# Performance work log

Hardware: AMD Instinct MI355X
Metric: run time of the kernel (lower is better)

Reference implementation:

```python
import jax, jax.numpy as jnp
import numpy as np

B, C, H, W = 8, 192, 56, 56
OUT, K = 192, 9
BN_EPS = 1e-5


def _l2_normalize(x, axis):
    # matches torch F.normalize: x / max(||x||, eps)
    n = jnp.sqrt(jnp.sum(x * x, axis=axis, keepdims=True))
    return x / jnp.maximum(n, 1e-12)


def _knn_idx(x_bnc, k):
    # dense pairwise squared distances, then k nearest (includes self)
    sq = jnp.sum(x_bnc * x_bnc, axis=-1, keepdims=True)            # (b,n,1)
    dist = sq - 2.0 * jnp.einsum('bnc,bmc->bnm', x_bnc, x_bnc) + jnp.swapaxes(sq, 1, 2)
    _, idx = jax.lax.top_k(-dist, k)                                # (b,n,k)
    return idx


def setup_inputs() -> dict:
    key = jax.random.key(0)
    k1, k2 = jax.random.split(key)
    fan_in = 2 * C
    return {
        'x': jax.random.normal(k1, (B, C, H, W), dtype=jnp.float32),
        'conv_w': jax.random.normal(k2, (OUT, 2 * C), dtype=jnp.float32) * np.sqrt(2.0 / fan_in),
        'conv_b': jnp.zeros((OUT,), dtype=jnp.float32),
        'bn_gamma': jnp.ones((OUT,), dtype=jnp.float32),
        'bn_beta': jnp.zeros((OUT,), dtype=jnp.float32),
    }


def reference(x, conv_w, conv_b, bn_gamma, bn_beta):
    b, c, h, w = x.shape
    n = h * w
    xf = x.reshape(b, c, n)                      # (b,c,n) node features
    xt = jnp.swapaxes(xf, 1, 2)                  # (b,n,c)

    # graph build on L2-normalized features (torch does this under no_grad)
    xn = _l2_normalize(xt, axis=-1)
    idx = _knn_idx(jax.lax.stop_gradient(xn), K)  # (b,n,K) neighbor ids

    # gather neighbors; center gather is identity (center_idx == arange)
    x_j = jnp.take_along_axis(xt[:, :, None, :], idx[..., None], axis=1)  # (b,n,K,c)
    x_i = xt[:, :, None, :]                                               # (b,n,1,c)
    feat = jnp.concatenate([jnp.broadcast_to(x_i, x_j.shape), x_j - x_i], axis=-1)  # (b,n,K,2c)

    # 1x1 conv == per-edge linear
    y = jnp.einsum('bnke,oe->bnko', feat, conv_w) + conv_b                # (b,n,K,out)

    # BatchNorm2d (training-mode batch stats over b,n,K per channel)
    mean = jnp.mean(y, axis=(0, 1, 2))
    var = jnp.var(y, axis=(0, 1, 2))
    y = (y - mean) * jax.lax.rsqrt(var + BN_EPS) * bn_gamma + bn_beta

    y = jax.nn.gelu(y, approximate=False)
    y = jnp.max(y, axis=2)                        # max over K neighbors -> (b,n,out)
    return jnp.transpose(y, (0, 2, 1)).reshape(b, -1, h, w)
```

## Files before the change

### kernel.cpp

```cpp
#include <hip/hip_runtime.h>
#include <hip/hip_bf16.h>
#include <math.h>

#define BB 8
#define CC 192
#define HH 56
#define WW 56
#define NPTS 3136
#define OUTC 192
#define KNN 9
#define NTILES 49
#define NCH 2
#define NT4 98
#define NBLK4 (NT4 * BB)

typedef __bf16 bf16x8 __attribute__((ext_vector_type(8)));
typedef float  f32x16 __attribute__((ext_vector_type(16)));

__device__ __forceinline__ unsigned short f2bf(float f) {
    unsigned u = __float_as_uint(f);
    u += 0x7fffu + ((u >> 16) & 1u);
    return (unsigned short)(u >> 16);
}
__device__ __forceinline__ float bf2f(unsigned short h) {
    return __uint_as_float(((unsigned)h) << 16);
}
__device__ __forceinline__ float gelu_f(float z) {
    return 0.5f * z * (1.0f + erff(z * 0.70710678118654752f));
}

__device__ __forceinline__ void ins12u32(unsigned (&t)[12], unsigned key) {
    if (key >= t[11]) return;
    t[11] = key;
#pragma unroll
    for (int q = 11; q > 0; --q) {
        const unsigned a = t[q-1], bq = t[q];
        const bool sw = bq < a;
        t[q-1] = sw ? bq : a;
        t[q]   = sw ? a : bq;
    }
}

__device__ __forceinline__ void ins12u(unsigned long long (&t)[12], unsigned long long key) {
    if (key >= t[11]) return;
    t[11] = key;
#pragma unroll
    for (int q = 11; q > 0; --q) {
        const unsigned long long a = t[q-1], bq = t[q];
        const bool sw = bq < a;
        t[q-1] = sw ? bq : a;
        t[q]   = sw ? a : bq;
    }
}

__device__ __forceinline__ void ins9f(float (&d)[9], int (&ix)[9], float nd, int ni) {
    if (!((nd < d[8]) || (nd == d[8] && ni < ix[8]))) return;
    d[8] = nd; ix[8] = ni;
#pragma unroll
    for (int q = 8; q > 0; --q) {
        if ((d[q] < d[q-1]) || (d[q] == d[q-1] && ix[q] < ix[q-1])) {
            float t = d[q]; d[q] = d[q-1]; d[q-1] = t;
            int t2 = ix[q]; ix[q] = ix[q-1]; ix[q-1] = t2;
        }
    }
}

__global__ __launch_bounds__(256) void k1_normalize(const float* __restrict__ x,
                                                    float* __restrict__ xn,
                                                    unsigned short* __restrict__ xh,
                                                    unsigned short* __restrict__ xl,
                                                    float* __restrict__ normv,
                                                    float* __restrict__ sqv) {
    const int b  = blockIdx.y;
    const int n0 = blockIdx.x * 64;
    __shared__ float tile[64 * 193];
    __shared__ float red[4][64];
    __shared__ float inv[64];
    const int tid = threadIdx.x;
    const int p   = tid & 63;
    const int cg  = tid >> 6;
    const float* xb = x + (size_t)b * CC * NPTS;

    float acc = 0.f;
#pragma unroll 4
    for (int t = 0; t < 48; ++t) {
        const int c = cg * 48 + t;
        const float v = xb[(size_t)c * NPTS + n0 + p];
        tile[p * 193 + c] = v;
        acc += v * v;
    }
    red[cg][p] = acc;
    __syncthreads();
    if (cg == 0) {
        const float s  = red[0][p] + red[1][p] + red[2][p] + red[3][p];
        float nc = sqrtf(s);
        nc = fmaxf(nc, 1e-12f);
        normv[b * NPTS + n0 + p] = nc;
        const float iv = 1.0f / nc;
        inv[p] = iv;
        sqv[b * NPTS + n0 + p] = s * iv * iv;
    }
    __syncthreads();
    const size_t base = ((size_t)b * NPTS + n0) * CC;
    float* dst = xn + base;
    for (int q = tid; q < 64 * CC / 4; q += 256) {
        const int f   = q * 4;
        const int row = f / CC;
        const int c   = f - row * CC;
        const float iv = inv[row];
        float4 v;
        v.x = tile[row * 193 + c + 0] * iv;
        v.y = tile[row * 193 + c + 1] * iv;
        v.z = tile[row * 193 + c + 2] * iv;
        v.w = tile[row * 193 + c + 3] * iv;
        *(float4*)&dst[f] = v;
        ushort4 hv, lv;
        hv.x = f2bf(v.x); lv.x = f2bf(v.x - bf2f(hv.x));
        hv.y = f2bf(v.y); lv.y = f2bf(v.y - bf2f(hv.y));
        hv.z = f2bf(v.z); lv.z = f2bf(v.z - bf2f(hv.z));
        hv.w = f2bf(v.w); lv.w = f2bf(v.w - bf2f(hv.w));
        *(ushort4*)&xh[base + f] = hv;
        *(ushort4*)&xl[base + f] = lv;
    }
}

__global__ __launch_bounds__(256, 3) void k2_knn(const unsigned short* __restrict__ xh,
                                                 const unsigned short* __restrict__ xl,
                                                 unsigned long long* __restrict__ pd) {
    const int b     = blockIdx.x;
    const int chunk = blockIdx.y;
    const int r0    = blockIdx.z * 64;
    const int t0    = chunk ? 25 : 0;
    const int t1    = chunk ? 49 : 25;

    __shared__ __align__(16) unsigned short Cs[64 * 200];
    __shared__ unsigned long long cdu[4][64][12];

    const int tid  = threadIdx.x;
    const int w    = tid >> 6;
    const int lane = tid & 63;
    const int wc   = w & 1;
    const int wr   = w >> 1;
    const int l31  = lane & 31;
    const int lhi  = lane >> 5;
    const int koffe = lhi * 8;
    const int myrow = wc * 32 + l31;

    const size_t rbase = ((size_t)b * NPTS + (r0 + myrow)) * CC;
    bf16x8 Rh[12], Rl[12];
#pragma unroll
    for (int c = 0; c < 12; ++c) {
        Rh[c] = *(const bf16x8*)(const void*)(xh + rbase + c * 16 + koffe);
        Rl[c] = *(const bf16x8*)(const void*)(xl + rbase + c * 16 + koffe);
    }

    unsigned t12[12];
#pragma unroll
    for (int q = 0; q < 12; ++q) t12[q] = 0xFFFFFFFFu;

    const int cfb = (wr * 32 + l31) * 200 + koffe;

    for (int ct = t0; ct < t1; ++ct) {
        const int c0 = ct * 64;
        __syncthreads();
#pragma unroll
        for (int rep = 0; rep < 6; ++rep) {
            const int cidx  = rep * 256 + tid;
            const int point = cidx / 24;
            const int c8    = cidx - point * 24;
            *(uint4*)(void*)&Cs[point * 200 + c8 * 8] =
                *(const uint4*)(const void*)(xh + ((size_t)b * NPTS + c0 + point) * CC + c8 * 8);
        }
        __syncthreads();

        f32x16 acc;
#pragma unroll
        for (int r = 0; r < 16; ++r) acc[r] = 0.f;

#pragma unroll
        for (int c = 0; c < 12; ++c) {
            const bf16x8 cf = *(const bf16x8*)(const void*)&Cs[cfb + c * 16];
            acc = __builtin_amdgcn_mfma_f32_32x32x16_bf16(cf, Rh[c], acc, 0, 0, 0);
            acc = __builtin_amdgcn_mfma_f32_32x32x16_bf16(cf, Rl[c], acc, 0, 0, 0);
        }
        __syncthreads();
#pragma unroll
        for (int rep = 0; rep < 6; ++rep) {
            const int cidx  = rep * 256 + tid;
            const int point = cidx / 24;
            const int c8    = cidx - point * 24;
            *(uint4*)(void*)&Cs[point * 200 + c8 * 8] =
                *(const uint4*)(const void*)(xl + ((size_t)b * NPTS + c0 + point) * CC + c8 * 8);
        }
        __syncthreads();
#pragma unroll
        for (int c = 0; c < 12; ++c) {
            const bf16x8 cl = *(const bf16x8*)(const void*)&Cs[cfb + c * 16];
            acc = __builtin_amdgcn_mfma_f32_32x32x16_bf16(cl, Rh[c], acc, 0, 0, 0);
        }

        const unsigned tbase = (unsigned)((ct - t0) << 4);
#pragma unroll
        for (int reg = 0; reg < 16; ++reg) {
            const float d = fmaxf(1.0f - acc[reg], 0.0f);
            const unsigned key = (__float_as_uint(d) & 0xFFFFFE00u) | (tbase | (unsigned)reg);
            ins12u32(t12, key);
        }
    }

#pragma unroll
    for (int q = 0; q < 12; ++q) {
        const unsigned key = t12[q];
        const int tag = (int)(key & 511u);
        const int reg = tag & 15;
        const int col = (t0 + (tag >> 4)) * 64 + wr * 32 + ((reg & 3) + 8 * (reg >> 2) + 4 * lhi);
        cdu[wr * 2 + lhi][myrow][q] = ((unsigned long long)key << 32) | (unsigned)col;
    }
    __syncthreads();
    if (tid < 64) {
        unsigned long long t[12];
#pragma unroll
        for (int q = 0; q < 12; ++q) t[q] = cdu[0][tid][q];
        for (int s = 1; s < 4; ++s)
#pragma unroll
            for (int q = 0; q < 12; ++q) ins12u(t, cdu[s][tid][q]);
        const size_t gbase = ((size_t)b * NPTS + r0 + tid) * (NCH * 12) + chunk * 12;
#pragma unroll
        for (int q = 0; q < 12; ++q) pd[gbase + q] = t[q];
    }
}

__global__ __launch_bounds__(128) void k2b_merge(const float* __restrict__ xn,
                                                 const float* __restrict__ sqv,
                                                 const unsigned long long* __restrict__ pd,
                                                 int* __restrict__ idxout) {
    const int b  = blockIdx.x;
    const int r0 = blockIdx.y * 32;
    __shared__ __align__(16) float xr_s[32][196];
    __shared__ int   ci[32][12];
    __shared__ float dd[32][13];
    __shared__ int   need[32];
    const int tid = threadIdx.x;
    const float* xb = xn + (size_t)b * NPTS * CC;

    for (int q = tid; q < 32 * 48; q += 128) {
        const int row = q / 48, c4 = q - row * 48;
        *(float4*)&xr_s[row][c4 * 4] = *(const float4*)&xb[(size_t)(r0 + row) * CC + c4 * 4];
    }
    if (tid < 32) {
        const size_t base = ((size_t)b * NPTS + r0 + tid) * (NCH * 12);
        unsigned long long t[12];
#pragma unroll
        for (int q = 0; q < 12; ++q) t[q] = pd[base + q];
        for (int s = 1; s < NCH; ++s)
#pragma unroll
            for (int q = 0; q < 12; ++q) ins12u(t, pd[base + s * 12 + q]);
#pragma unroll
        for (int q = 0; q < 12; ++q) ci[tid][q] = (int)(t[q] & 0xFFFFFFFFull);
        const float d9  = __uint_as_float((unsigned)(t[8] >> 32) & 0xFFFFFE00u);
        const float d10 = __uint_as_float((unsigned)(t[9] >> 32) & 0xFFFFFE00u);
        need[tid] = (d10 - d9) < 3e-4f ? 1 : 0;
    }
    __syncthreads();
    {
        const int p = tid >> 2;
        const int s = tid & 3;
        if (need[p]) {
            const float sqn = sqv[(size_t)b * NPTS + r0 + p];
#pragma unroll
            for (int t3 = 0; t3 < 3; ++t3) {
                const int cs2 = s + t3 * 4;
                const int m   = ci[p][cs2];
                const float* xm = xb + (size_t)m * CC;
                float4 a4 = make_float4(0.f, 0.f, 0.f, 0.f);
#pragma unroll 8
                for (int c4 = 0; c4 < 48; ++c4) {
                    const float4 xv = *(const float4*)&xm[c4 * 4];
                    const float4 rv = *(const float4*)&xr_s[p][c4 * 4];
                    a4.x += rv.x * xv.x;
                    a4.y += rv.y * xv.y;
                    a4.z += rv.z * xv.z;
                    a4.w += rv.w * xv.w;
                }
                const float dot = (a4.x + a4.y) + (a4.z + a4.w);
                dd[p][cs2] = sqn + sqv[(size_t)b * NPTS + m] - 2.0f * dot;
            }
        }
    }
    __syncthreads();
    if (tid < 32) {
        int* orow = &idxout[((size_t)b * NPTS + r0 + tid) * KNN];
        if (need[tid]) {
            float fd[9]; int fi[9];
#pragma unroll
            for (int q = 0; q < 9; ++q) { fd[q] = 3.4e38f; fi[q] = 0x7fffffff; }
#pragma unroll
            for (int cs2 = 0; cs2 < 12; ++cs2)
                ins9f(fd, fi, dd[tid][cs2], ci[tid][cs2]);
#pragma unroll
            for (int q = 0; q < 9; ++q) orow[q] = fi[q];
        } else {
#pragma unroll
            for (int q = 0; q < 9; ++q) orow[q] = ci[tid][q];
        }
    }
}

__global__ __launch_bounds__(256) void k3a_wcat(const float* __restrict__ cw,
                                               unsigned short* __restrict__ wh,
                                               unsigned short* __restrict__ wl) {
    const int i = blockIdx.x * 256 + threadIdx.x;
    if (i < 2 * OUTC * CC) {
        const int r = i / CC, c = i - r * CC;
        float val;
        if (r < OUTC) val = cw[r * (2 * CC) + c] - cw[r * (2 * CC) + CC + c];
        else          val = cw[(r - OUTC) * (2 * CC) + CC + c];
        const unsigned short h = f2bf(val);
        wh[i] = h;
        wl[i] = f2bf(val - bf2f(h));
    }
}

__global__ __launch_bounds__(256) void k3_mfma(const unsigned short* __restrict__ xh,
                                               const unsigned short* __restrict__ xl,
                                               const unsigned short* __restrict__ wh,
                                               const unsigned short* __restrict__ wl,
                                               const float* __restrict__ normv,
                                               const float* __restrict__ conv_b,
                                               float* __restrict__ uv) {
    const int m0 = blockIdx.x * 64;
    const int o0 = blockIdx.y * 64;
    const int tid  = threadIdx.x;
    const int w    = tid >> 6;
    const int lane = tid & 63;
    const int wr   = w >> 1;
    const int wc   = w & 1;
    const int l31  = lane & 31;
    const int lhi  = lane >> 5;
    const int koffe = lhi * 8;

    const size_t abase = (size_t)(m0 + wr * 32 + l31) * CC;
    bf16x8 Ah[12], Al[12];
#pragma unroll
    for (int c = 0; c < 12; ++c) {
        Ah[c] = *(const bf16x8*)(const void*)(xh + abase + c * 16 + koffe);
        Al[c] = *(const bf16x8*)(const void*)(xl + abase + c * 16 + koffe);
    }
    const int o = o0 + wc * 32 + l31;
    const unsigned short* whr = wh + (size_t)o * CC;
    const unsigned short* wlr = wl + (size_t)o * CC;

    f32x16 acc;
#pragma unroll
    for (int r = 0; r < 16; ++r) acc[r] = 0.f;
#pragma unroll
    for (int c = 0; c < 12; ++c) {
        const bf16x8 bh = *(const bf16x8*)(const void*)(whr + c * 16 + koffe);
        const bf16x8 bl = *(const bf16x8*)(const void*)(wlr + c * 16 + koffe);
        acc = __builtin_amdgcn_mfma_f32_32x32x16_bf16(Ah[c], bh, acc, 0, 0, 0);
        acc = __builtin_amdgcn_mfma_f32_32x32x16_bf16(Al[c], bh, acc, 0, 0, 0);
        acc = __builtin_amdgcn_mfma_f32_32x32x16_bf16(Ah[c], bl, acc, 0, 0, 0);
    }
    const float bias = (o < OUTC) ? conv_b[o] : 0.0f;
#pragma unroll
    for (int reg = 0; reg < 16; ++reg) {
        const int m = m0 + wr * 32 + (reg & 3) + 8 * (reg >> 2) + 4 * lhi;
        uv[(size_t)m * (2 * OUTC) + o] = acc[reg] * normv[m] + bias;
    }
}

__global__ __launch_bounds__(256) void k4_fused(const float* __restrict__ uv,
                                                const int* __restrict__ idxb,
                                                float* __restrict__ amax,
                                                float* __restrict__ amin,
                                                float* __restrict__ partials) {
    const int flat = blockIdx.x;
    const int b    = flat & 7;
    const int tile = flat >> 3;
    const int tid  = threadIdx.x;
    const int p    = tid >> 3;
    const int g    = tid & 7;
    const int n    = tile * 32 + p;
    const size_t base = (size_t)b * NPTS;
    __shared__ float red[256 * 25];

    float sv[24], sv2[24], vmx[24], vmn[24];
#pragma unroll
    for (int c = 0; c < 24; ++c) { sv[c] = 0.f; sv2[c] = 0.f; vmx[c] = -3.4e38f; vmn[c] = 3.4e38f; }

    const int* ix = &idxb[(base + n) * KNN];
#pragma unroll
    for (int k = 0; k < KNN; ++k) {
        const int m = ix[k];
        const float* vr = &uv[(base + m) * (2 * OUTC) + OUTC + g * 24];
#pragma unroll
        for (int c4 = 0; c4 < 6; ++c4) {
            const float4 v = *(const float4*)&vr[c4 * 4];
            const int c = c4 * 4;
            sv[c+0] += v.x; sv2[c+0] += v.x*v.x; vmx[c+0] = fmaxf(vmx[c+0], v.x); vmn[c+0] = fminf(vmn[c+0], v.x);
            sv[c+1] += v.y; sv2[c+1] += v.y*v.y; vmx[c+1] = fmaxf(vmx[c+1], v.y); vmn[c+1] = fminf(vmn[c+1], v.y);
            sv[c+2] += v.z; sv2[c+2] += v.z*v.z; vmx[c+2] = fmaxf(vmx[c+2], v.z); vmn[c+2] = fminf(vmn[c+2], v.z);
            sv[c+3] += v.w; sv2[c+3] += v.w*v.w; vmx[c+3] = fmaxf(vmx[c+3], v.w); vmn[c+3] = fminf(vmn[c+3], v.w);
        }
    }
    const float* ur = &uv[(base + n) * (2 * OUTC) + g * 24];
    float S[24], Q[24];
    float* am = &amax[(base + n) * OUTC + g * 24];
    float* an = &amin[(base + n) * OUTC + g * 24];
#pragma unroll
    for (int c4 = 0; c4 < 6; ++c4) {
        const float4 u4 = *(const float4*)&ur[c4 * 4];
        const int c = c4 * 4;
        float4 mx, mn;
        mx.x = u4.x + vmx[c+0]; mn.x = u4.x + vmn[c+0];
        mx.y = u4.y + vmx[c+1]; mn.y = u4.y + vmn[c+1];
        mx.z = u4.z + vmx[c+2]; mn.z = u4.z + vmn[c+2];
        mx.w = u4.w + vmx[c+3]; mn.w = u4.w + vmn[c+3];
        *(float4*)&am[c4 * 4] = mx;
        *(float4*)&an[c4 * 4] = mn;
        S[c+0] = 9.f*u4.x + sv[c+0];  Q[c+0] = u4.x*(9.f*u4.x + 2.f*sv[c+0]) + sv2[c+0];
        S[c+1] = 9.f*u4.y + sv[c+1];  Q[c+1] = u4.y*(9.f*u4.y + 2.f*sv[c+1]) + sv2[c+1];
        S[c+2] = 9.f*u4.z + sv[c+2];  Q[c+2] = u4.z*(9.f*u4.z + 2.f*sv[c+2]) + sv2[c+2];
        S[c+3] = 9.f*u4.w + sv[c+3];  Q[c+3] = u4.w*(9.f*u4.w + 2.f*sv[c+3]) + sv2[c+3];
    }
#pragma unroll
    for (int c = 0; c < 24; ++c) red[tid * 25 + c] = S[c];
    __syncthreads();
    float accS = 0.f;
    if (tid < OUTC) {
        const int go = tid / 24, co = tid - go * 24;
        for (int pp = 0; pp < 32; ++pp) accS += red[(pp * 8 + go) * 25 + co];
    }
    __syncthreads();
#pragma unroll
    for (int c = 0; c < 24; ++c) red[tid * 25 + c] = Q[c];
    __syncthreads();
    if (tid < OUTC) {
        const int go = tid / 24, co = tid - go * 24;
        float accQ = 0.f;
        for (int pp = 0; pp < 32; ++pp) accQ += red[(pp * 8 + go) * 25 + co];
        partials[(size_t)flat * (2 * OUTC) + tid]        = accS;
        partials[(size_t)flat * (2 * OUTC) + OUTC + tid] = accQ;
    }
}

__global__ __launch_bounds__(192) void k4b_finalize(const float* __restrict__ partials,
                                                    const float* __restrict__ gamma,
                                                    const float* __restrict__ beta,
                                                    float* __restrict__ scsh) {
    const int o = threadIdx.x;
    float S = 0.f, Q = 0.f;
    for (int blk = 0; blk < NBLK4; ++blk) {
        S += partials[(size_t)blk * (2 * OUTC) + o];
        Q += partials[(size_t)blk * (2 * OUTC) + OUTC + o];
    }
    const float cnt  = (float)BB * (float)NPTS * (float)KNN;
    const float mean = S / cnt;
    float var = Q / cnt - mean * mean;
    var = fmaxf(var, 0.0f);
    const float scale = gamma[o] * rsqrtf(var + 1e-5f);
    scsh[o]        = scale;
    scsh[OUTC + o] = beta[o] - mean * scale;
}

__global__ __launch_bounds__(256) void k5_out(const float* __restrict__ amax,
                                              const float* __restrict__ amin,
                                              const float* __restrict__ scsh,
                                              float* __restrict__ out) {
    const int b  = blockIdx.y;
    const int n0 = blockIdx.x * 64;
    __shared__ float zb[64 * 193];
    __shared__ float ssc[OUTC];
    __shared__ float ssh[OUTC];
    const int tid = threadIdx.x;
    for (int q = tid; q < OUTC; q += 256) {
        ssc[q] = scsh[q];
        ssh[q] = scsh[OUTC + q];
    }
    __syncthreads();
    const int p  = tid >> 2;
    const int og = tid & 3;
    const int n  = n0 + p;
    const size_t rb = ((size_t)b * NPTS + n) * OUTC + og * 48;
#pragma unroll
    for (int t4 = 0; t4 < 12; ++t4) {
        const float4 ax = *(const float4*)&amax[rb + t4 * 4];
        const float4 an = *(const float4*)&amin[rb + t4 * 4];
        const int ob = og * 48 + t4 * 4;
        float z1, z2;
        z1 = ax.x * ssc[ob+0] + ssh[ob+0]; z2 = an.x * ssc[ob+0] + ssh[ob+0];
        zb[p * 193 + ob + 0] = fmaxf(gelu_f(z1), gelu_f(z2));
        z1 = ax.y * ssc[ob+1] + ssh[ob+1]; z2 = an.y * ssc[ob+1] + ssh[ob+1];
        zb[p * 193 + ob + 1] = fmaxf(gelu_f(z1), gelu_f(z2));
        z1 = ax.z * ssc[ob+2] + ssh[ob+2]; z2 = an.z * ssc[ob+2] + ssh[ob+2];
        zb[p * 193 + ob + 2] = fmaxf(gelu_f(z1), gelu_f(z2));
        z1 = ax.w * ssc[ob+3] + ssh[ob+3]; z2 = an.w * ssc[ob+3] + ssh[ob+3];
        zb[p * 193 + ob + 3] = fmaxf(gelu_f(z1), gelu_f(z2));
    }
    __syncthreads();
    float* ob2 = out + (size_t)b * OUTC * NPTS;
    for (int q = tid; q < 64 * OUTC; q += 256) {
        const int o  = q >> 6;
        const int pp = q & 63;
        ob2[(size_t)o * NPTS + n0 + pp] = zb[pp * 193 + o];
    }
}

extern "C" void kernel_launch(void* const* d_in, const int* in_sizes, int n_in,
                              void* d_out, int out_size, void* d_ws, size_t ws_size,
                              hipStream_t stream) {
    const float* x        = (const float*)d_in[0];
    const float* conv_w   = (const float*)d_in[1];
    const float* conv_b   = (const float*)d_in[2];
    const float* bn_gamma = (const float*)d_in[3];
    const float* bn_beta  = (const float*)d_in[4];
    float* out = (float*)d_out;

    float* ws = (float*)d_ws;
    const size_t SZ_XN = (size_t)BB * NPTS * CC;
    const size_t SZ_NV = (size_t)BB * NPTS;
    const size_t SZ_A  = (size_t)BB * NPTS * OUTC;

    int*   idxb        = (int*)ws;
    unsigned short* wh = (unsigned short*)(idxb + (size_t)BB * NPTS * KNN);
    unsigned short* wl = wh + (size_t)(2 * OUTC) * CC;
    float* uv       = (float*)(wl + (size_t)(2 * OUTC) * CC);
    float* partials = uv + (size_t)BB * NPTS * (2 * OUTC);
    float* scsh     = partials + (size_t)NBLK4 * (2 * OUTC);
    float* normv    = scsh + 2 * OUTC;
    float* sqv      = normv + SZ_NV;
    float* xn       = sqv + SZ_NV;
    unsigned short* xh = (unsigned short*)(xn + SZ_XN);
    unsigned short* xl = xh + SZ_XN;
    unsigned long long* pd = (unsigned long long*)uv;
    float* amax = xn;
    float* amin = xn + SZ_A;

    k1_normalize<<<dim3(NTILES, BB), 256, 0, stream>>>(x, xn, xh, xl, normv, sqv);
    k2_knn<<<dim3(BB, NCH, NTILES), 256, 0, stream>>>(xh, xl, pd);
    k2b_merge<<<dim3(BB, NT4), 128, 0, stream>>>(xn, sqv, pd, idxb);
    k3a_wcat<<<(2 * OUTC * CC + 255) / 256, 256, 0, stream>>>(conv_w, wh, wl);
    k3_mfma<<<dim3(BB * NPTS / 64, (2 * OUTC) / 64), 256, 0, stream>>>(xh, xl, wh, wl, normv, conv_b, uv);
    k4_fused<<<NBLK4, 256, 0, stream>>>(uv, idxb, amax, amin, partials);
    k4b_finalize<<<1, 192, 0, stream>>>(partials, bn_gamma, bn_beta, scsh);
    k5_out<<<dim3(NTILES, BB), 256, 0, stream>>>(amax, amin, scsh, out);
}
```

Baseline: 422.8 us.

## Move half of KNN row fragments to LDS and parallelize BN finalize

In the KNN kernel, the row operand fragments for the second half of the channels (hi and lo parts) are now staged in shared memory instead of being held in registers. This cuts register pressure so more waves can stay resident, and the shared buffer is reused for the candidate merge area. The candidate tile loads are also reindexed so each group of four threads copies one point. Separately, the BN finalize kernel goes from one block that serially sums all partials to one block per channel with a tree reduction. The cost is extra LDS reads in the inner MFMA loop and one more barrier.

```diff
diff --git a/kernel.cpp b/kernel.cpp
--- a/kernel.cpp
+++ b/kernel.cpp
@@ -16,6 +16,7 @@
 
 typedef __bf16 bf16x8 __attribute__((ext_vector_type(8)));
 typedef float  f32x16 __attribute__((ext_vector_type(16)));
+typedef int    i32x4  __attribute__((ext_vector_type(4)));
 
 __device__ __forceinline__ unsigned short f2bf(float f) {
     unsigned u = __float_as_uint(f);
@@ -133,8 +134,10 @@
     const int t0    = chunk ? 25 : 0;
     const int t1    = chunk ? 49 : 25;
 
-    __shared__ __align__(16) unsigned short Cs[64 * 200];
-    __shared__ unsigned long long cdu[4][64][12];
+    __shared__ __align__(16) char smem[51200];
+    unsigned short* Cs  = (unsigned short*)smem;
+    unsigned short* Rk1 = (unsigned short*)(smem + 25600);
+    unsigned long long* cdu = (unsigned long long*)smem;
 
     const int tid  = threadIdx.x;
     const int w    = tid >> 6;
@@ -146,12 +149,31 @@
     const int koffe = lhi * 8;
     const int myrow = wc * 32 + l31;
 
+    const int spnt = tid >> 2;
+    const int sj   = tid & 3;
+
     const size_t rbase = ((size_t)b * NPTS + (r0 + myrow)) * CC;
-    bf16x8 Rh[12], Rl[12];
-#pragma unroll
-    for (int c = 0; c < 12; ++c) {
-        Rh[c] = *(const bf16x8*)(const void*)(xh + rbase + c * 16 + koffe);
-        Rl[c] = *(const bf16x8*)(const void*)(xl + rbase + c * 16 + koffe);
+    bf16x8 Rh0[6], Rl0[6];
+#pragma unroll
+    for (int c = 0; c < 6; ++c) {
+        Rh0[c] = *(const bf16x8*)(const void*)(xh + rbase + c * 16 + koffe);
+        Rl0[c] = *(const bf16x8*)(const void*)(xl + rbase + c * 16 + koffe);
+    }
+
+    {
+        const size_t pb = ((size_t)b * NPTS + r0 + spnt) * CC + 96;
+#pragma unroll
+        for (int rep = 0; rep < 3; ++rep) {
+            const int j = sj + rep * 4;
+            *(uint4*)(void*)&Rk1[spnt * 200 + j * 8] =
+                *(const uint4*)(const void*)(xh + pb + j * 8);
+        }
+#pragma unroll
+        for (int rep = 0; rep < 3; ++rep) {
+            const int j = sj + rep * 4;
+            *(uint4*)(void*)&Rk1[spnt * 200 + 96 + j * 8] =
+                *(const uint4*)(const void*)(xl + pb + j * 8);
+        }
     }
 
     unsigned t12[12];
@@ -159,17 +181,19 @@
     for (int q = 0; q < 12; ++q) t12[q] = 0xFFFFFFFFu;
 
     const int cfb = (wr * 32 + l31) * 200 + koffe;
+    const int rlb = myrow * 200 + koffe;
 
     for (int ct = t0; ct < t1; ++ct) {
         const int c0 = ct * 64;
         __syncthreads();
-#pragma unroll
-        for (int rep = 0; rep < 6; ++rep) {
-            const int cidx  = rep * 256 + tid;
-            const int point = cidx / 24;
-            const int c8    = cidx - point * 24;
-            *(uint4*)(void*)&Cs[point * 200 + c8 * 8] =
-                *(const uint4*)(const void*)(xh + ((size_t)b * NPTS + c0 + point) * CC + c8 * 8);
+        {
+            const size_t pb = ((size_t)b * NPTS + c0 + spnt) * CC;
+#pragma unroll
+            for (int rep = 0; rep < 6; ++rep) {
+                const int j = sj + rep * 4;
+                *(uint4*)(void*)&Cs[spnt * 200 + j * 8] =
+                    *(const uint4*)(const void*)(xh + pb + j * 8);
+            }
         }
         __syncthreads();
 
@@ -178,25 +202,40 @@
         for (int r = 0; r < 16; ++r) acc[r] = 0.f;
 
 #pragma unroll
-        for (int c = 0; c < 12; ++c) {
+        for (int c = 0; c < 6; ++c) {
             const bf16x8 cf = *(const bf16x8*)(const void*)&Cs[cfb + c * 16];
-            acc = __builtin_amdgcn_mfma_f32_32x32x16_bf16(cf, Rh[c], acc, 0, 0, 0);
-            acc = __builtin_amdgcn_mfma_f32_32x32x16_bf16(cf, Rl[c], acc, 0, 0, 0);
+            acc = __builtin_amdgcn_mfma_f32_32x32x16_bf16(cf, Rh0[c], acc, 0, 0, 0);
+            acc = __builtin_amdgcn_mfma_f32_32x32x16_bf16(cf, Rl0[c], acc, 0, 0, 0);
+        }
+#pragma unroll
+        for (int c = 0; c < 6; ++c) {
+            const bf16x8 cf = *(const bf16x8*)(const void*)&Cs[cfb + (6 + c) * 16];
+            const i32x4 th = *(const volatile i32x4*)(const volatile void*)&Rk1[rlb + c * 16];
+            const i32x4 tl = *(const volatile i32x4*)(const volatile void*)&Rk1[rlb + 96 + c * 16];
+            acc = __builtin_amdgcn_mfma_f32_32x32x16_bf16(cf, __builtin_bit_cast(bf16x8, th), acc, 0, 0, 0);
+            acc = __builtin_amdgcn_mfma_f32_32x32x16_bf16(cf, __builtin_bit_cast(bf16x8, tl), acc, 0, 0, 0);
         }
         __syncthreads();
-#pragma unroll
-        for (int rep = 0; rep < 6; ++rep) {
-            const int cidx  = rep * 256 + tid;
-            const int point = cidx / 24;
-            const int c8    = cidx - point * 24;
-            *(uint4*)(void*)&Cs[point * 200 + c8 * 8] =
-                *(const uint4*)(const void*)(xl + ((size_t)b * NPTS + c0 + point) * CC + c8 * 8);
+        {
+            const size_t pb = ((size_t)b * NPTS + c0 + spnt) * CC;
+#pragma unroll
+            for (int rep = 0; rep < 6; ++rep) {
+                const int j = sj + rep * 4;
+                *(uint4*)(void*)&Cs[spnt * 200 + j * 8] =
+                    *(const uint4*)(const void*)(xl + pb + j * 8);
+            }
         }
         __syncthreads();
 #pragma unroll
-        for (int c = 0; c < 12; ++c) {
+        for (int c = 0; c < 6; ++c) {
             const bf16x8 cl = *(const bf16x8*)(const void*)&Cs[cfb + c * 16];
-            acc = __builtin_amdgcn_mfma_f32_32x32x16_bf16(cl, Rh[c], acc, 0, 0, 0);
+            acc = __builtin_amdgcn_mfma_f32_32x32x16_bf16(cl, Rh0[c], acc, 0, 0, 0);
+        }
+#pragma unroll
+        for (int c = 0; c < 6; ++c) {
+            const bf16x8 cl = *(const bf16x8*)(const void*)&Cs[cfb + (6 + c) * 16];
+            const i32x4 th = *(const volatile i32x4*)(const volatile void*)&Rk1[rlb + c * 16];
+            acc = __builtin_amdgcn_mfma_f32_32x32x16_bf16(cl, __builtin_bit_cast(bf16x8, th), acc, 0, 0, 0);
         }
 
         const unsigned tbase = (unsigned)((ct - t0) << 4);
@@ -208,22 +247,23 @@
         }
     }
 
+    __syncthreads();
 #pragma unroll
     for (int q = 0; q < 12; ++q) {
         const unsigned key = t12[q];
         const int tag = (int)(key & 511u);
         const int reg = tag & 15;
         const int col = (t0 + (tag >> 4)) * 64 + wr * 32 + ((reg & 3) + 8 * (reg >> 2) + 4 * lhi);
-        cdu[wr * 2 + lhi][myrow][q] = ((unsigned long long)key << 32) | (unsigned)col;
+        cdu[(((wr * 2 + lhi) * 64) + myrow) * 12 + q] = ((unsigned long long)key << 32) | (unsigned)col;
     }
     __syncthreads();
     if (tid < 64) {
         unsigned long long t[12];
 #pragma unroll
-        for (int q = 0; q < 12; ++q) t[q] = cdu[0][tid][q];
+        for (int q = 0; q < 12; ++q) t[q] = cdu[tid * 12 + q];
         for (int s = 1; s < 4; ++s)
 #pragma unroll
-            for (int q = 0; q < 12; ++q) ins12u(t, cdu[s][tid][q]);
+            for (int q = 0; q < 12; ++q) ins12u(t, cdu[(s * 64 + tid) * 12 + q]);
         const size_t gbase = ((size_t)b * NPTS + r0 + tid) * (NCH * 12) + chunk * 12;
 #pragma unroll
         for (int q = 0; q < 12; ++q) pd[gbase + q] = t[q];
@@ -444,23 +484,32 @@
     }
 }
 
-__global__ __launch_bounds__(192) void k4b_finalize(const float* __restrict__ partials,
+__global__ __launch_bounds__(256) void k4b_finalize(const float* __restrict__ partials,
                                                     const float* __restrict__ gamma,
                                                     const float* __restrict__ beta,
                                                     float* __restrict__ scsh) {
-    const int o = threadIdx.x;
+    const int o   = blockIdx.x;
+    const int tid = threadIdx.x;
+    __shared__ float sS[256], sQ[256];
     float S = 0.f, Q = 0.f;
-    for (int blk = 0; blk < NBLK4; ++blk) {
+    for (int blk = tid; blk < NBLK4; blk += 256) {
         S += partials[(size_t)blk * (2 * OUTC) + o];
         Q += partials[(size_t)blk * (2 * OUTC) + OUTC + o];
     }
-    const float cnt  = (float)BB * (float)NPTS * (float)KNN;
-    const float mean = S / cnt;
-    float var = Q / cnt - mean * mean;
-    var = fmaxf(var, 0.0f);
-    const float scale = gamma[o] * rsqrtf(var + 1e-5f);
-    scsh[o]        = scale;
-    scsh[OUTC + o] = beta[o] - mean * scale;
+    sS[tid] = S; sQ[tid] = Q;
+    __syncthreads();
+    for (int s = 128; s > 0; s >>= 1) {
+        if (tid < s) { sS[tid] += sS[tid + s]; sQ[tid] += sQ[tid + s]; }
+        __syncthreads();
+    }
+    if (tid == 0) {
+        const float cnt  = (float)BB * (float)NPTS * (float)KNN;
+        const float mean = sS[0] / cnt;
+        float var = fmaxf(sQ[0] / cnt - mean * mean, 0.0f);
+        const float scale = gamma[o] * rsqrtf(var + 1e-5f);
+        scsh[o]        = scale;
+        scsh[OUTC + o] = beta[o] - mean * scale;
+    }
 }
 
 __global__ __launch_bounds__(256) void k5_out(const float* __restrict__ amax,
@@ -542,6 +591,6 @@
     k3a_wcat<<<(2 * OUTC * CC + 255) / 256, 256, 0, stream>>>(conv_w, wh, wl);
     k3_mfma<<<dim3(BB * NPTS / 64, (2 * OUTC) / 64), 256, 0, stream>>>(xh, xl, wh, wl, normv, conv_b, uv);
     k4_fused<<<NBLK4, 256, 0, stream>>>(uv, idxb, amax, amin, partials);
-    k4b_finalize<<<1, 192, 0, stream>>>(partials, bn_gamma, bn_beta, scsh);
+    k4b_finalize<<<OUTC, 256, 0, stream>>>(partials, bn_gamma, bn_beta, scsh);
     k5_out<<<dim3(NTILES, BB), 256, 0, stream>>>(amax, amin, scsh, out);
 }
```

Measured after the change: 388.6 us. -8.1%, faster.
